# Kernel tuning notes

Hardware: AMD Instinct MI355X
Metric: run time of the kernel (lower is better)

Reference implementation:

```python
import jax, jax.numpy as jnp
import numpy as np

N, XDIM, D, K = 400000, 128, 3, 4
TWO_PI = 2.0 * np.pi


def _scaled(k, shape):
    fan_in = shape[0]
    return jax.random.normal(k, shape, jnp.float32) * np.float32(1.0 / np.sqrt(fan_in))


def setup_inputs() -> dict:
    key = jax.random.key(0)
    ks = jax.random.split(key, 9)
    return {
        "x1": jax.random.normal(ks[0], (N, XDIM), jnp.float32),
        "enc_w1": _scaled(ks[1], (XDIM, 16)), "enc_b1": jnp.zeros((16,), jnp.float32),
        "enc_w2": _scaled(ks[2], (16, 8)),   "enc_b2": jnp.zeros((8,), jnp.float32),
        "enc_w3": _scaled(ks[3], (8, 1)),    "enc_b3": jnp.zeros((1,), jnp.float32),
        "dec_w1": _scaled(ks[4], (1, 8)),    "dec_b1": jnp.zeros((8,), jnp.float32),
        "dec_w2": _scaled(ks[5], (8, 16)),   "dec_b2": jnp.zeros((16,), jnp.float32),
        "dec_w3": _scaled(ks[6], (16, XDIM)),"dec_b3": jnp.zeros((XDIM,), jnp.float32),
        "est_w1": _scaled(ks[7], (D, 8)),    "est_b1": jnp.zeros((8,), jnp.float32),
        "est_w2": _scaled(ks[8], (8, K)),    "est_b2": jnp.zeros((K,), jnp.float32),
    }


def reference(x1, enc_w1, enc_b1, enc_w2, enc_b2, enc_w3, enc_b3,
              dec_w1, dec_b1, dec_w2, dec_b2, dec_w3, dec_b3,
              est_w1, est_b1, est_w2, est_b2):
    # encoder: Dense(16,tanh)->Dense(8,tanh)->Dense(1,tanh)
    h = jnp.tanh(x1 @ enc_w1 + enc_b1)
    h = jnp.tanh(h @ enc_w2 + enc_b2)
    z1 = jnp.tanh(h @ enc_w3 + enc_b3)            # [N,1]
    # decoder: Dense(8,tanh)->Dense(16,tanh)->Dense(xdim, linear)
    h = jnp.tanh(z1 @ dec_w1 + dec_b1)
    h = jnp.tanh(h @ dec_w2 + dec_b2)
    x2 = h @ dec_w3 + dec_b3                      # [N,xdim]

    # relative distances
    dist_cos = jnp.sum(x1 * x2, axis=1, keepdims=True) / (
        jnp.linalg.norm(x1, axis=1, keepdims=True) * jnp.linalg.norm(x2, axis=1, keepdims=True))
    dist_euc = jnp.linalg.norm(x1 - x2, axis=1, keepdims=True)
    z = jnp.concatenate([z1, dist_cos, dist_euc], axis=1)   # [N,D]

    # estimator: Dense(8,tanh)->Dense(K,softmax)
    gamma = jax.nn.softmax(jnp.tanh(z @ est_w1 + est_b1) @ est_w2 + est_b2)  # [N,K]

    # GMM parameters from soft assignments
    gamma_sum = jnp.sum(gamma, axis=0)                        # [K]
    phi = jnp.mean(gamma, axis=0)                             # [K]
    mu = jnp.einsum('ik,il->kl', gamma, z) / gamma_sum[:, None]          # [K,D]
    z_centered = jnp.sqrt(gamma)[:, :, None] * (z[:, None, :] - mu[None, :, :])  # [N,K,D]
    sigma = jnp.einsum('ikl,ikm->klm', z_centered, z_centered) / gamma_sum[:, None, None]  # [K,D,D]

    # per-sample energy
    z_mu = z[:, None, :] - mu[None, :, :]                     # [N,K,D]
    sigma_inv = jnp.linalg.inv(sigma)                         # [K,D,D]
    item1 = jnp.log(phi)[None, :]                             # [1,K]
    item2 = -0.5 * jnp.einsum('nkd,kde,nke->nk', z_mu, sigma_inv, z_mu)  # [N,K]
    sigma_det = jnp.linalg.det(TWO_PI * sigma)                # [K]
    item3 = jnp.log(jnp.sqrt(sigma_det))[None, :]             # [1,K]
    energy = -jnp.sum(item1 + item2 - item3, axis=1)          # [N]

    # loss
    lambda1, lambda2 = 0.01, 0.0001
    diag = jnp.diagonal(sigma, axis1=-2, axis2=-1)            # [K,D]
    loss3 = lambda2 * jnp.sum(1.0 / diag)
    loss2 = lambda1 * jnp.mean(energy)
    loss1 = jnp.mean(jnp.sum(jnp.square(x1 - x2), axis=1))
    loss = loss1 + loss2 + loss3
    return energy, loss
```

## Files before the change

kernel.cpp:

```cpp
#include <hip/hip_runtime.h>

#define NSAMP 400000
#define NBLK  1563


__device__ __forceinline__ float ftanh(float x) {
    float e = __expf(2.0f * x);
    return 1.0f - __fdividef(2.0f, e + 1.0f);
}

__global__ __launch_bounds__(256) void prep_kernel(const float* __restrict__ dw3,
                                                   const float* __restrict__ db3,
                                                   float* __restrict__ Gm,
                                                   float* __restrict__ gv,
                                                   float* __restrict__ bb) {
    __shared__ float sw3[2048];
    __shared__ float sb3[128];
    int t = threadIdx.x;
    for (int k = t; k < 2048; k += 256) sw3[k] = dw3[k];
    if (t < 128) sb3[t] = db3[t];
    __syncthreads();
    int a = t >> 4, b = t & 15;
    float s = 0.f;
    for (int j = 0; j < 128; ++j) s = fmaf(sw3[a * 128 + j], sw3[b * 128 + j], s);
    Gm[t] = s;
    if (t < 16) {
        float sg = 0.f;
        for (int j = 0; j < 128; ++j) sg = fmaf(sw3[t * 128 + j], sb3[j], sg);
        gv[t] = sg;
    }
    if (t == 0) {
        float sbv = 0.f;
        for (int j = 0; j < 128; ++j) sbv = fmaf(sb3[j], sb3[j], sbv);
        *bb = sbv;
    }
}

__global__ __launch_bounds__(256) void pass1_kernel(
    const float* __restrict__ x1,
    const float* __restrict__ ew1, const float* __restrict__ eb1,
    const float* __restrict__ ew2, const float* __restrict__ eb2,
    const float* __restrict__ ew3, const float* __restrict__ eb3,
    const float* __restrict__ dw1, const float* __restrict__ db1,
    const float* __restrict__ dw2, const float* __restrict__ db2,
    const float* __restrict__ dw3, const float* __restrict__ db3,
    const float* __restrict__ tw1, const float* __restrict__ tb1,
    const float* __restrict__ tw2, const float* __restrict__ tb2,
    const float* __restrict__ Gm, const float* __restrict__ gv,
    const float* __restrict__ bbp,
    double* __restrict__ acc, float4* __restrict__ zbuf) {
    __shared__ float4 lbuf[1024];
    __shared__ float sPart[4][41];

    int t = threadIdx.x;
    int i = blockIdx.x * 256 + t;
    bool active = (i < NSAMP);
    int bbase = blockIdx.x * 256;
    int w = t >> 6, lane = t & 63;
    int sw2 = (t >> 1) & 3;
    const float4* x1f4 = (const float4*)x1;

    float u[16], v[16];
#pragma unroll
    for (int k = 0; k < 16; ++k) { u[k] = 0.f; v[k] = 0.f; }
    float s2 = 0.f, sb = 0.f;

#pragma unroll 1
    for (int blk = 0; blk < 8; ++blk) {
#pragma unroll
        for (int c2 = 0; c2 < 4; ++c2) {
            int idx = (w * 4 + c2) * 64 + lane;
            int row = idx >> 2, qs = idx & 3;
            int q = qs ^ ((row >> 1) & 3);
            int grow = bbase + row;
            if (grow >= NSAMP) grow = NSAMP - 1;
            const float4* src = x1f4 + (size_t)grow * 32 + blk * 4 + q;
            float4* dst = lbuf + (w * 4 + c2) * 64;
            __builtin_amdgcn_global_load_lds(
                (const __attribute__((address_space(1))) void*)src,
                (__attribute__((address_space(3))) void*)dst, 16, 0, 0);
        }
        __syncthreads();

        float xe[16];
#pragma unroll
        for (int q = 0; q < 4; ++q) {
            float4 w4 = lbuf[t * 4 + (q ^ sw2)];
            xe[q * 4 + 0] = w4.x; xe[q * 4 + 1] = w4.y;
            xe[q * 4 + 2] = w4.z; xe[q * 4 + 3] = w4.w;
        }
        int j0 = blk * 16;
#pragma unroll
        for (int e = 0; e < 16; ++e) {
            float x = xe[e];
            s2 = fmaf(x, x, s2);
            sb = fmaf(x, db3[j0 + e], sb);
#pragma unroll
            for (int k = 0; k < 16; ++k) u[k] = fmaf(x, ew1[(j0 + e) * 16 + k], u[k]);
        }
#pragma unroll
        for (int q = 0; q < 16; ++q) {
            float a2 = v[q];
#pragma unroll
            for (int e = 0; e < 16; ++e) a2 = fmaf(xe[e], dw3[q * 128 + j0 + e], a2);
            v[q] = a2;
        }
        __syncthreads();
    }

    float h1[16];
#pragma unroll
    for (int k = 0; k < 16; ++k) h1[k] = ftanh(u[k] + eb1[k]);
    float h2[8];
#pragma unroll
    for (int m = 0; m < 8; ++m) {
        float a2 = eb2[m];
#pragma unroll
        for (int k = 0; k < 16; ++k) a2 = fmaf(h1[k], ew2[k * 8 + m], a2);
        h2[m] = ftanh(a2);
    }
    float a3 = eb3[0];
#pragma unroll
    for (int m = 0; m < 8; ++m) a3 = fmaf(h2[m], ew3[m], a3);
    float z1 = ftanh(a3);

    float d1[8];
#pragma unroll
    for (int p = 0; p < 8; ++p) d1[p] = ftanh(fmaf(z1, dw1[p], db1[p]));
    float d2[16];
#pragma unroll
    for (int q = 0; q < 16; ++q) {
        float a2 = db2[q];
#pragma unroll
        for (int p = 0; p < 8; ++p) a2 = fmaf(d1[p], dw2[p * 16 + q], a2);
        d2[q] = ftanh(a2);
    }

    float dot = sb;
#pragma unroll
    for (int q = 0; q < 16; ++q) dot = fmaf(d2[q], v[q], dot);
    float n2 = *bbp;
#pragma unroll
    for (int a = 0; a < 16; ++a) {
        float ra = 2.0f * gv[a];
#pragma unroll
        for (int b = 0; b < 16; ++b) ra = fmaf(Gm[a * 16 + b], d2[b], ra);
        n2 = fmaf(d2[a], ra, n2);
    }
    n2 = fmaxf(n2, 1e-20f);
    float euc2 = fmaxf(s2 - 2.0f * dot + n2, 0.f);
    float deuc = sqrtf(euc2);
    float dcos = dot * rsqrtf(s2 * n2);

    float zf[3] = {z1, dcos, deuc};

    float e1[8];
#pragma unroll
    for (int p = 0; p < 8; ++p) {
        float a2 = tb1[p];
        a2 = fmaf(zf[0], tw1[0 * 8 + p], a2);
        a2 = fmaf(zf[1], tw1[1 * 8 + p], a2);
        a2 = fmaf(zf[2], tw1[2 * 8 + p], a2);
        e1[p] = ftanh(a2);
    }
    float lg[4];
#pragma unroll
    for (int k = 0; k < 4; ++k) {
        float a2 = tb2[k];
#pragma unroll
        for (int p = 0; p < 8; ++p) a2 = fmaf(e1[p], tw2[p * 4 + k], a2);
        lg[k] = a2;
    }
    float mx = fmaxf(fmaxf(lg[0], lg[1]), fmaxf(lg[2], lg[3]));
    float ex[4]; float se = 0.f;
#pragma unroll
    for (int k = 0; k < 4; ++k) { ex[k] = __expf(lg[k] - mx); se += ex[k]; }
    float inv = __fdividef(1.0f, se);
    float gam[4];
#pragma unroll
    for (int k = 0; k < 4; ++k) gam[k] = ex[k] * inv;

    if (active) zbuf[i] = make_float4(zf[0], zf[1], zf[2], 0.f);
    if (!active) { gam[0] = gam[1] = gam[2] = gam[3] = 0.f; euc2 = 0.f; }

    int rlane = threadIdx.x & 63;
    int wid = threadIdx.x >> 6;

#define REDUCE_STORE(T, VAL) { float _v = (VAL);                          \
        _v += __shfl_down(_v, 32); _v += __shfl_down(_v, 16);             \
        _v += __shfl_down(_v, 8);  _v += __shfl_down(_v, 4);              \
        _v += __shfl_down(_v, 2);  _v += __shfl_down(_v, 1);              \
        if (rlane == 0) sPart[wid][T] = _v; }

#pragma unroll
    for (int k = 0; k < 4; ++k) REDUCE_STORE(k, gam[k]);
#pragma unroll
    for (int k = 0; k < 4; ++k) {
#pragma unroll
        for (int d = 0; d < 3; ++d) REDUCE_STORE(4 + k * 3 + d, gam[k] * zf[d]);
    }
#pragma unroll
    for (int k = 0; k < 4; ++k) {
        REDUCE_STORE(16 + k * 6 + 0, gam[k] * zf[0] * zf[0]);
        REDUCE_STORE(16 + k * 6 + 1, gam[k] * zf[0] * zf[1]);
        REDUCE_STORE(16 + k * 6 + 2, gam[k] * zf[0] * zf[2]);
        REDUCE_STORE(16 + k * 6 + 3, gam[k] * zf[1] * zf[1]);
        REDUCE_STORE(16 + k * 6 + 4, gam[k] * zf[1] * zf[2]);
        REDUCE_STORE(16 + k * 6 + 5, gam[k] * zf[2] * zf[2]);
    }
    REDUCE_STORE(40, euc2);
#undef REDUCE_STORE

    __syncthreads();
    if (threadIdx.x < 41) {
        double s = (double)sPart[0][threadIdx.x] + (double)sPart[1][threadIdx.x]
                 + (double)sPart[2][threadIdx.x] + (double)sPart[3][threadIdx.x];
        unsafeAtomicAdd(&acc[threadIdx.x], s);
    }
}

__global__ void gmm_kernel(double* __restrict__ acc, float* __restrict__ P) {
    if (threadIdx.x != 0 || blockIdx.x != 0) return;
    double M[6] = {0, 0, 0, 0, 0, 0}, bv[3] = {0, 0, 0}, A = 0.0, loss3 = 0.0;
    const double TWO_PI = 6.283185307179586;
    for (int k = 0; k < 4; ++k) {
        double g = acc[k];
        double phi = g / (double)NSAMP;
        double mu0 = acc[4 + k * 3 + 0] / g;
        double mu1 = acc[4 + k * 3 + 1] / g;
        double mu2 = acc[4 + k * 3 + 2] / g;
        double S00 = acc[16 + k * 6 + 0] / g - mu0 * mu0;
        double S01 = acc[16 + k * 6 + 1] / g - mu0 * mu1;
        double S02 = acc[16 + k * 6 + 2] / g - mu0 * mu2;
        double S11 = acc[16 + k * 6 + 3] / g - mu1 * mu1;
        double S12 = acc[16 + k * 6 + 4] / g - mu1 * mu2;
        double S22 = acc[16 + k * 6 + 5] / g - mu2 * mu2;
        double c00 = S11 * S22 - S12 * S12;
        double c01 = S02 * S12 - S01 * S22;
        double c02 = S01 * S12 - S02 * S11;
        double det = S00 * c00 + S01 * c01 + S02 * c02;
        double id = 1.0 / det;
        double I00 = c00 * id, I01 = c01 * id, I02 = c02 * id;
        double I11 = (S00 * S22 - S02 * S02) * id;
        double I12 = (S01 * S02 - S00 * S12) * id;
        double I22 = (S00 * S11 - S01 * S01) * id;
        M[0] += I00; M[1] += I01; M[2] += I02; M[3] += I11; M[4] += I12; M[5] += I22;
        double b0 = I00 * mu0 + I01 * mu1 + I02 * mu2;
        double b1 = I01 * mu0 + I11 * mu1 + I12 * mu2;
        double b2 = I02 * mu0 + I12 * mu1 + I22 * mu2;
        bv[0] += b0; bv[1] += b1; bv[2] += b2;
        double quad = mu0 * b0 + mu1 * b1 + mu2 * b2;
        A += -log(phi) + 0.5 * log(TWO_PI * TWO_PI * TWO_PI * det) + 0.5 * quad;
        loss3 += 1e-4 * (1.0 / S00 + 1.0 / S11 + 1.0 / S22);
    }
    P[0] = (float)M[0]; P[1] = (float)M[1]; P[2] = (float)M[2];
    P[3] = (float)M[3]; P[4] = (float)M[4]; P[5] = (float)M[5];
    P[6] = (float)bv[0]; P[7] = (float)bv[1]; P[8] = (float)bv[2];
    P[9] = (float)A;
    acc[42] = acc[40] / (double)NSAMP + loss3;
}

__global__ __launch_bounds__(256) void energy_kernel(const float4* __restrict__ zbuf,
                                                     const float* __restrict__ P,
                                                     double* __restrict__ acc,
                                                     unsigned* __restrict__ cnt,
                                                     float* __restrict__ out) {
    int i = blockIdx.x * 256 + threadIdx.x;
    float e = 0.f;
    if (i < NSAMP) {
        float4 z4 = zbuf[i];
        float z0 = z4.x, z1 = z4.y, z2 = z4.z;
        float q = P[0] * z0 * z0 + P[3] * z1 * z1 + P[5] * z2 * z2
                + 2.f * (P[1] * z0 * z1 + P[2] * z0 * z2 + P[4] * z1 * z2);
        e = P[9] + 0.5f * q - (P[6] * z0 + P[7] * z1 + P[8] * z2);
        out[i] = e;
    }
    float s = e;
    s += __shfl_down(s, 32); s += __shfl_down(s, 16); s += __shfl_down(s, 8);
    s += __shfl_down(s, 4);  s += __shfl_down(s, 2);  s += __shfl_down(s, 1);
    __shared__ float sE[4];
    if ((threadIdx.x & 63) == 0) sE[threadIdx.x >> 6] = s;
    __syncthreads();
    if (threadIdx.x == 0) {
        double t = (double)sE[0] + (double)sE[1] + (double)sE[2] + (double)sE[3];
        unsafeAtomicAdd(&acc[41], t);
        __threadfence();
        unsigned old = atomicAdd(cnt, 1u);
        if (old == (unsigned)(NBLK - 1)) {
            double tot = unsafeAtomicAdd(&acc[41], 0.0);
            out[NSAMP] = (float)(acc[42] + 0.01 * tot / (double)NSAMP);
        }
    }
}

extern "C" void kernel_launch(void* const* d_in, const int* in_sizes, int n_in,
                              void* d_out, int out_size, void* d_ws, size_t ws_size,
                              hipStream_t stream) {
    const float* x1  = (const float*)d_in[0];
    const float* ew1 = (const float*)d_in[1];
    const float* eb1 = (const float*)d_in[2];
    const float* ew2 = (const float*)d_in[3];
    const float* eb2 = (const float*)d_in[4];
    const float* ew3 = (const float*)d_in[5];
    const float* eb3 = (const float*)d_in[6];
    const float* dw1 = (const float*)d_in[7];
    const float* db1 = (const float*)d_in[8];
    const float* dw2 = (const float*)d_in[9];
    const float* db2 = (const float*)d_in[10];
    const float* dw3 = (const float*)d_in[11];
    const float* db3 = (const float*)d_in[12];
    const float* tw1 = (const float*)d_in[13];
    const float* tb1 = (const float*)d_in[14];
    const float* tw2 = (const float*)d_in[15];
    const float* tb2 = (const float*)d_in[16];
    float* out = (float*)d_out;
    char* ws = (char*)d_ws;
    double* acc   = (double*)ws;
    unsigned* cnt = (unsigned*)(ws + 352);
    float* P    = (float*)(ws + 384);
    float* Gm   = (float*)(ws + 1024);
    float* gv   = (float*)(ws + 2048);
    float* bb   = (float*)(ws + 2112);
    float4* zb  = (float4*)(ws + 4096);

    hipMemsetAsync(d_ws, 0, 512, stream);
    prep_kernel<<<1, 256, 0, stream>>>(dw3, db3, Gm, gv, bb);
    pass1_kernel<<<NBLK, 256, 0, stream>>>(x1, ew1, eb1, ew2, eb2, ew3, eb3,
                                           dw1, db1, dw2, db2, dw3, db3,
                                           tw1, tb1, tw2, tb2, Gm, gv, bb, acc, zb);
    gmm_kernel<<<1, 64, 0, stream>>>(acc, P);
    energy_kernel<<<NBLK, 256, 0, stream>>>(zb, P, acc, cnt, out);
}
```

Measured before the change: 472.9 us.

## Double-buffer x1 LDS staging and replace block barriers with per-wave vmcnt waits

```diff
diff --git a/kernel.cpp b/kernel.cpp
--- a/kernel.cpp
+++ b/kernel.cpp
@@ -49,7 +49,7 @@
     const float* __restrict__ Gm, const float* __restrict__ gv,
     const float* __restrict__ bbp,
     double* __restrict__ acc, float4* __restrict__ zbuf) {
-    __shared__ float4 lbuf[1024];
+    __shared__ float4 lbuf[2048];
     __shared__ float sPart[4][41];
 
     int t = threadIdx.x;
@@ -60,32 +60,36 @@
     int sw2 = (t >> 1) & 3;
     const float4* x1f4 = (const float4*)x1;
 
+    const float4* p[4];
+#pragma unroll
+    for (int c2 = 0; c2 < 4; ++c2) {
+        int idx = (w * 4 + c2) * 64 + lane;
+        int row = idx >> 2, qs = idx & 3;
+        int q = qs ^ ((row >> 1) & 3);
+        int grow = bbase + row;
+        if (grow >= NSAMP) grow = NSAMP - 1;
+        p[c2] = x1f4 + (size_t)grow * 32 + q;
+    }
+
+#pragma unroll
+    for (int c2 = 0; c2 < 4; ++c2) {
+        __builtin_amdgcn_global_load_lds(
+            (const __attribute__((address_space(1))) void*)p[c2],
+            (__attribute__((address_space(3))) void*)(lbuf + (w * 4 + c2) * 64),
+            16, 0, 0);
+        p[c2] += 4;
+    }
+
     float u[16], v[16];
 #pragma unroll
     for (int k = 0; k < 16; ++k) { u[k] = 0.f; v[k] = 0.f; }
     float s2 = 0.f, sb = 0.f;
 
-#pragma unroll 1
-    for (int blk = 0; blk < 8; ++blk) {
-#pragma unroll
-        for (int c2 = 0; c2 < 4; ++c2) {
-            int idx = (w * 4 + c2) * 64 + lane;
-            int row = idx >> 2, qs = idx & 3;
-            int q = qs ^ ((row >> 1) & 3);
-            int grow = bbase + row;
-            if (grow >= NSAMP) grow = NSAMP - 1;
-            const float4* src = x1f4 + (size_t)grow * 32 + blk * 4 + q;
-            float4* dst = lbuf + (w * 4 + c2) * 64;
-            __builtin_amdgcn_global_load_lds(
-                (const __attribute__((address_space(1))) void*)src,
-                (__attribute__((address_space(3))) void*)dst, 16, 0, 0);
-        }
-        __syncthreads();
-
+    auto consume = [&](int blk, int bofs) {
         float xe[16];
 #pragma unroll
         for (int q = 0; q < 4; ++q) {
-            float4 w4 = lbuf[t * 4 + (q ^ sw2)];
+            float4 w4 = lbuf[bofs + t * 4 + (q ^ sw2)];
             xe[q * 4 + 0] = w4.x; xe[q * 4 + 1] = w4.y;
             xe[q * 4 + 2] = w4.z; xe[q * 4 + 3] = w4.w;
         }
@@ -105,8 +109,26 @@
             for (int e = 0; e < 16; ++e) a2 = fmaf(xe[e], dw3[q * 128 + j0 + e], a2);
             v[q] = a2;
         }
-        __syncthreads();
-    }
+    };
+
+#pragma unroll 1
+    for (int blk = 0; blk < 7; ++blk) {
+        int nb = ((blk + 1) & 1) * 1024;
+#pragma unroll
+        for (int c2 = 0; c2 < 4; ++c2) {
+            __builtin_amdgcn_global_load_lds(
+                (const __attribute__((address_space(1))) void*)p[c2],
+                (__attribute__((address_space(3))) void*)(lbuf + nb + (w * 4 + c2) * 64),
+                16, 0, 0);
+            p[c2] += 4;
+        }
+        asm volatile("s_waitcnt vmcnt(4)" ::: "memory");
+        __builtin_amdgcn_sched_barrier(0);
+        consume(blk, (blk & 1) * 1024);
+    }
+    asm volatile("s_waitcnt vmcnt(0)" ::: "memory");
+    __builtin_amdgcn_sched_barrier(0);
+    consume(7, 1024);
 
     float h1[16];
 #pragma unroll
@@ -126,13 +148,13 @@
 
     float d1[8];
 #pragma unroll
-    for (int p = 0; p < 8; ++p) d1[p] = ftanh(fmaf(z1, dw1[p], db1[p]));
+    for (int p2 = 0; p2 < 8; ++p2) d1[p2] = ftanh(fmaf(z1, dw1[p2], db1[p2]));
     float d2[16];
 #pragma unroll
     for (int q = 0; q < 16; ++q) {
         float a2 = db2[q];
 #pragma unroll
-        for (int p = 0; p < 8; ++p) a2 = fmaf(d1[p], dw2[p * 16 + q], a2);
+        for (int p2 = 0; p2 < 8; ++p2) a2 = fmaf(d1[p2], dw2[p2 * 16 + q], a2);
         d2[q] = ftanh(a2);
     }
 
@@ -156,19 +178,19 @@
 
     float e1[8];
 #pragma unroll
-    for (int p = 0; p < 8; ++p) {
-        float a2 = tb1[p];
-        a2 = fmaf(zf[0], tw1[0 * 8 + p], a2);
-        a2 = fmaf(zf[1], tw1[1 * 8 + p], a2);
-        a2 = fmaf(zf[2], tw1[2 * 8 + p], a2);
-        e1[p] = ftanh(a2);
+    for (int p2 = 0; p2 < 8; ++p2) {
+        float a2 = tb1[p2];
+        a2 = fmaf(zf[0], tw1[0 * 8 + p2], a2);
+        a2 = fmaf(zf[1], tw1[1 * 8 + p2], a2);
+        a2 = fmaf(zf[2], tw1[2 * 8 + p2], a2);
+        e1[p2] = ftanh(a2);
     }
     float lg[4];
 #pragma unroll
     for (int k = 0; k < 4; ++k) {
         float a2 = tb2[k];
 #pragma unroll
-        for (int p = 0; p < 8; ++p) a2 = fmaf(e1[p], tw2[p * 4 + k], a2);
+        for (int p2 = 0; p2 < 8; ++p2) a2 = fmaf(e1[p2], tw2[p2 * 4 + k], a2);
         lg[k] = a2;
     }
     float mx = fmaxf(fmaxf(lg[0], lg[1]), fmaxf(lg[2], lg[3]));
```

Result: no change. 471.3 us (-0.3%).
